# Optimization experiments

Measured on AMD Instinct MI355X. Metric: run time of the kernel, lower is better.

The kernel has to match this reference:

```python
import jax, jax.numpy as jnp
import numpy as np

N = 50000      # nodes
E = 800000     # edges
IN = 256       # in_dim
HID = 64       # num_hidden
H0 = 4         # heads[0]
H1 = 1         # heads[1]
OUT1 = HID * H0  # 256, last GATConv out_feats
C = 64         # num_classes
NEG_SLOPE = 0.2


def setup_inputs() -> dict:
    ks = jax.random.split(jax.random.key(0), 13)
    s = 0.05
    return {
        "x":   jax.random.normal(ks[0], (N, IN), jnp.float32),
        "src": jax.random.randint(ks[1], (E,), 0, N, jnp.int32),
        "dst": jax.random.randint(ks[2], (E,), 0, N, jnp.int32),
        # layer 0: GATConv(IN, HID, H0)
        "W0":  jax.random.normal(ks[3], (IN, H0 * HID), jnp.float32) * s,
        "al0": jax.random.normal(ks[4], (H0, HID), jnp.float32) * s,
        "ar0": jax.random.normal(ks[5], (H0, HID), jnp.float32) * s,
        "b0":  jnp.zeros((H0 * HID,), jnp.float32),
        # layer 1: GATConv(H0*HID, OUT1, H1), residual (identity since in == H1*OUT1)
        "W1":  jax.random.normal(ks[6], (H0 * HID, H1 * OUT1), jnp.float32) * s,
        "al1": jax.random.normal(ks[7], (H1, OUT1), jnp.float32) * s,
        "ar1": jax.random.normal(ks[8], (H1, OUT1), jnp.float32) * s,
        "b1":  jnp.zeros((H1 * OUT1,), jnp.float32),
        # final classifier Linear(OUT1, C)
        "Wl":  jax.random.normal(ks[9], (OUT1, C), jnp.float32) * s,
        "bl":  jnp.zeros((C,), jnp.float32),
    }


def gat_conv(h, src, dst, W, al, ar, b, heads, out, residual, act):
    # ft: projected per-head features [N, H, D]
    ft = (h @ W).reshape(-1, heads, out)
    el = jnp.sum(ft * al, axis=-1)          # [N, H]
    er = jnp.sum(ft * ar, axis=-1)          # [N, H]
    e = jax.nn.leaky_relu(el[src] + er[dst], NEG_SLOPE)  # [E, H]
    # edge softmax grouped by destination node
    emax = jax.ops.segment_max(e, dst, num_segments=N)
    a = jnp.exp(e - emax[dst])
    asum = jax.ops.segment_sum(a, dst, num_segments=N)
    alpha = a / asum[dst]                   # [E, H]
    msg = alpha[:, :, None] * ft[src]       # [E, H, D]
    rst = jax.ops.segment_sum(msg, dst, num_segments=N)  # [N, H, D]
    if residual:  # identity residual (in_feats == heads*out)
        rst = rst + h.reshape(-1, heads, out)
    rst = rst + b.reshape(1, heads, out)
    if act is not None:
        rst = act(rst)
    return rst


def reference(x, src, dst, W0, al0, ar0, b0, W1, al1, ar1, b1, Wl, bl):
    h = gat_conv(x, src, dst, W0, al0, ar0, b0, H0, HID, False, jax.nn.elu)
    h = h.reshape(N, -1)                    # flatten(1) -> [N, H0*HID]
    h = gat_conv(h, src, dst, W1, al1, ar1, b1, H1, OUT1, True, None)
    h = h.mean(axis=1)                      # mean over heads -> [N, OUT1]
    logits = h @ Wl + bl
    return (logits, h)
```

## Files before the change

### kernel.cpp

```cpp
#include <hip/hip_runtime.h>
#include <hip/hip_bf16.h>
#include <stdint.h>

#define NNODES 50000
#define NEDGES 800000
#define CH     256
#define NCLS   64

typedef __attribute__((ext_vector_type(8))) short  short8;
typedef __attribute__((ext_vector_type(4))) float  floatx4;

__device__ __forceinline__ float bf2f(unsigned short u) {
    union { unsigned int i; float f; } v; v.i = ((unsigned int)u) << 16; return v.f;
}
__device__ __forceinline__ unsigned short f2bf(float f) {
    union { float f; unsigned int i; } v; v.f = f;
    unsigned int x = v.i;
    return (unsigned short)((x + 0x7fffu + ((x >> 16) & 1u)) >> 16);
}

__global__ void k_setup(const float* __restrict__ W0, const float* __restrict__ W1,
                        const float* __restrict__ Wl,
                        unsigned short* __restrict__ w0t, unsigned short* __restrict__ w1t,
                        unsigned short* __restrict__ wlt, int* __restrict__ deg) {
    int i = blockIdx.x * 256 + threadIdx.x;
    if (i < 65536) {
        int r = i >> 8, c = i & 255;
        w0t[c * 256 + r] = f2bf(W0[i]);
    } else if (i < 131072) {
        int j = i - 65536;
        int r = j >> 8, c = j & 255;
        w1t[c * 256 + r] = f2bf(W1[j]);
    } else if (i < 147456) {
        int j = i - 131072;
        int r = j >> 6, c = j & 63;
        wlt[c * 256 + r] = f2bf(Wl[j]);
    } else if (i < 147456 + NNODES) {
        deg[i - 147456] = 0;
    }
}

__global__ void k_hist(const int* __restrict__ dst, int* __restrict__ deg) {
    int e = blockIdx.x * 256 + threadIdx.x;
    if (e < NEDGES) {
        int d = dst[e];
        if ((unsigned)d < NNODES) atomicAdd(&deg[d], 1);
    }
}

__global__ void k_scan1(const int* __restrict__ in, int* __restrict__ out,
                        int* __restrict__ part, int n) {
    __shared__ int sm[256];
    int i = blockIdx.x * 256 + threadIdx.x;
    int v = (i < n) ? in[i] : 0;
    sm[threadIdx.x] = v;
    __syncthreads();
    for (int off = 1; off < 256; off <<= 1) {
        int t = (threadIdx.x >= (unsigned)off) ? sm[threadIdx.x - off] : 0;
        __syncthreads();
        sm[threadIdx.x] += t;
        __syncthreads();
    }
    if (i < n) out[i] = sm[threadIdx.x];
    if (threadIdx.x == 255) part[blockIdx.x] = sm[255];
}

__global__ void k_scan3(const int* __restrict__ scn, const int* __restrict__ deg,
                        const int* __restrict__ part, int* __restrict__ offs,
                        int* __restrict__ cursor, int n) {
    int i = blockIdx.x * 256 + threadIdx.x;
    if (i < n) {
        int add = (blockIdx.x > 0) ? part[blockIdx.x - 1] : 0;
        int o = scn[i] - deg[i] + add;
        offs[i] = o; cursor[i] = o;
    }
}

__global__ void k_scatter(const int* __restrict__ dst, const int* __restrict__ src,
                          int* __restrict__ cursor, int* __restrict__ esrc) {
    int e = blockIdx.x * 256 + threadIdx.x;
    if (e < NEDGES) {
        int d = dst[e];
        if ((unsigned)d < NNODES) {
            int p = atomicAdd(&cursor[d], 1);
            if ((unsigned)p < NEDGES) esrc[p] = src[e];
        }
    }
}

template<int BN, bool ABF16, bool OUTF32>
__global__ __launch_bounds__(256) void k_gemm(const void* __restrict__ Av,
                                              const unsigned short* __restrict__ BT,
                                              const float* __restrict__ bias,
                                              float* __restrict__ Cf,
                                              unsigned short* __restrict__ Cb,
                                              int M, int N) {
    constexpr int BK  = 32;
    constexpr int NT  = BN / 16;
    constexpr int LDA = BK + 8;
    __shared__ unsigned short As[128][LDA];
    __shared__ unsigned short Bs[BN][LDA];
    const int t  = threadIdx.x;
    const int w  = t >> 6, l = t & 63;
    const int lm = l & 15, lk = (l >> 4) * 8;
    const int m0 = blockIdx.x * 128;
    const int n0 = blockIdx.y * BN;
    const float* Af = (const float*)Av;
    const unsigned short* Ab = (const unsigned short*)Av;

    floatx4 acc[2][NT];
#pragma unroll
    for (int mt = 0; mt < 2; ++mt)
#pragma unroll
        for (int nt = 0; nt < NT; ++nt) acc[mt][nt] = (floatx4)0.0f;

    for (int k0 = 0; k0 < 256; k0 += BK) {
        if (ABF16) {
#pragma unroll
            for (int p = 0; p < 2; ++p) {
                int chunk = t + p * 256;
                int r = chunk >> 2, cc = (chunk & 3) * 8;
                int row = m0 + r;
                uint4 val = make_uint4(0, 0, 0, 0);
                if (row < M) val = *(const uint4*)(Ab + (size_t)row * 256 + k0 + cc);
                *(uint4*)&As[r][cc] = val;
            }
        } else {
#pragma unroll
            for (int p = 0; p < 4; ++p) {
                int chunk = t + p * 256;
                int r = chunk >> 3, cc = (chunk & 7) * 4;
                int row = m0 + r;
                float4 v = make_float4(0.f, 0.f, 0.f, 0.f);
                if (row < M) v = *(const float4*)(Af + (size_t)row * 256 + k0 + cc);
                ushort4 o; o.x = f2bf(v.x); o.y = f2bf(v.y); o.z = f2bf(v.z); o.w = f2bf(v.w);
                *(ushort4*)&As[r][cc] = o;
            }
        }
#pragma unroll
        for (int p = 0; p < (BN * 4) / 256; ++p) {
            int chunk = t + p * 256;
            int r = chunk >> 2, cc = (chunk & 3) * 8;
            *(uint4*)&Bs[r][cc] = *(const uint4*)(BT + (size_t)(n0 + r) * 256 + k0 + cc);
        }
        __syncthreads();
        short8 af0 = *(const short8*)&As[w * 32 +      lm][lk];
        short8 af1 = *(const short8*)&As[w * 32 + 16 + lm][lk];
#pragma unroll
        for (int nt = 0; nt < NT; ++nt) {
            short8 bf = *(const short8*)&Bs[nt * 16 + lm][lk];
            acc[0][nt] = __builtin_amdgcn_mfma_f32_16x16x32_bf16(af0, bf, acc[0][nt], 0, 0, 0);
            acc[1][nt] = __builtin_amdgcn_mfma_f32_16x16x32_bf16(af1, bf, acc[1][nt], 0, 0, 0);
        }
        __syncthreads();
    }
#pragma unroll
    for (int mt = 0; mt < 2; ++mt)
#pragma unroll
        for (int j = 0; j < 4; ++j) {
            int row = m0 + w * 32 + mt * 16 + (l >> 4) * 4 + j;
            if (row < M) {
#pragma unroll
                for (int nt = 0; nt < NT; ++nt) {
                    int gcol = n0 + nt * 16 + lm;
                    float v = acc[mt][nt][j];
                    if (bias) v += bias[gcol];
                    if (OUTF32) Cf[(size_t)row * N + gcol] = v;
                    else        Cb[(size_t)row * N + gcol] = f2bf(v);
                }
            }
        }
}

template<int H>
__global__ void k_el_er(const unsigned short* __restrict__ ft,
                        const float* __restrict__ al, const float* __restrict__ ar,
                        float* __restrict__ el, float* __restrict__ er) {
    constexpr int D = CH / H;
    constexpr int G = D / 4;
    int n = blockIdx.x * 4 + (threadIdx.x >> 6);
    int l = threadIdx.x & 63;
    int c = 4 * l;
    int h = c / D;
    ushort4 f = *(const ushort4*)(ft + (size_t)n * CH + c);
    float4 a = *(const float4*)(al + c);
    float4 b = *(const float4*)(ar + c);
    float f0 = bf2f(f.x), f1 = bf2f(f.y), f2 = bf2f(f.z), f3 = bf2f(f.w);
    float sl = f0 * a.x + f1 * a.y + f2 * a.z + f3 * a.w;
    float sr = f0 * b.x + f1 * b.y + f2 * b.z + f3 * b.w;
#pragma unroll
    for (int m = 1; m < G; m <<= 1) {
        sl += __shfl_xor(sl, m, 64);
        sr += __shfl_xor(sr, m, 64);
    }
    if ((l & (G - 1)) == 0) {
        el[n * H + h] = sl;
        er[n * H + h] = sr;
    }
}

template<int H, bool ELU, bool RESID>
__global__ __launch_bounds__(256) void k_agg(const unsigned short* __restrict__ ft,
                      const float* __restrict__ el, const float* __restrict__ er,
                      const int* __restrict__ offs, const int* __restrict__ deg,
                      const int* __restrict__ esrc,
                      const unsigned short* __restrict__ resid16,
                      const float* __restrict__ bias,
                      unsigned short* __restrict__ out_bf,
                      float* __restrict__ out_f) {
    constexpr int D = CH / H;
    constexpr int SLOTS = 64 / H;
    __shared__ float swgt[4][64];
    __shared__ int   ssrc[4][64];
    int w = threadIdx.x >> 6;
    int n = blockIdx.x * 4 + w;
    int l = threadIdx.x & 63;
    int c = 4 * l;
    int h = c / D;
    int slot = l / H, head = l & (H - 1);
    float ern1 = er[n * H + head];
    int st = offs[n], dg = deg[n];
    if (st < 0 || dg < 0 || st > NEDGES || dg > NEDGES - st) dg = 0;
    float a0 = 0.f, a1 = 0.f, a2 = 0.f, a3 = 0.f, ssum = 0.f;

    for (int i = 0; i < dg; i += SLOTS) {
        int idx = i + slot;
        int sv = 0; float wv = 0.f;
        if (idx < dg) {
            sv = esrc[st + idx];
            float xv = el[sv * H + head] + ern1;
            xv = (xv > 0.f) ? xv : 0.2f * xv;
            xv = fminf(xv, 60.f);
            wv = __expf(xv);
        }
        swgt[w][slot * H + head] = wv;
        if (head == 0) ssrc[w][slot] = sv;
        int jmax = dg - i; if (jmax > SLOTS) jmax = SLOTS;
        int j = 0;
        for (; j + 4 <= jmax; j += 4) {
            float w0 = swgt[w][(j + 0) * H + h], w1 = swgt[w][(j + 1) * H + h];
            float w2 = swgt[w][(j + 2) * H + h], w3 = swgt[w][(j + 3) * H + h];
            int s0 = ssrc[w][j + 0], s1 = ssrc[w][j + 1];
            int s2 = ssrc[w][j + 2], s3 = ssrc[w][j + 3];
            ushort4 f0 = *(const ushort4*)(ft + (size_t)s0 * CH + c);
            ushort4 f1 = *(const ushort4*)(ft + (size_t)s1 * CH + c);
            ushort4 f2 = *(const ushort4*)(ft + (size_t)s2 * CH + c);
            ushort4 f3 = *(const ushort4*)(ft + (size_t)s3 * CH + c);
            ssum += (w0 + w1) + (w2 + w3);
            a0 += w0 * bf2f(f0.x) + w1 * bf2f(f1.x) + w2 * bf2f(f2.x) + w3 * bf2f(f3.x);
            a1 += w0 * bf2f(f0.y) + w1 * bf2f(f1.y) + w2 * bf2f(f2.y) + w3 * bf2f(f3.y);
            a2 += w0 * bf2f(f0.z) + w1 * bf2f(f1.z) + w2 * bf2f(f2.z) + w3 * bf2f(f3.z);
            a3 += w0 * bf2f(f0.w) + w1 * bf2f(f1.w) + w2 * bf2f(f2.w) + w3 * bf2f(f3.w);
        }
        for (; j < jmax; ++j) {
            float wj = swgt[w][j * H + h];
            int sj = ssrc[w][j];
            ushort4 f = *(const ushort4*)(ft + (size_t)sj * CH + c);
            ssum += wj;
            a0 += wj * bf2f(f.x); a1 += wj * bf2f(f.y);
            a2 += wj * bf2f(f.z); a3 += wj * bf2f(f.w);
        }
    }
    float inv = (ssum > 1e-30f) ? 1.0f / ssum : 0.0f;
    a0 *= inv; a1 *= inv; a2 *= inv; a3 *= inv;
    if (RESID) {
        ushort4 r = *(const ushort4*)(resid16 + (size_t)n * CH + c);
        a0 += bf2f(r.x); a1 += bf2f(r.y); a2 += bf2f(r.z); a3 += bf2f(r.w);
    }
    {
        float4 b = *(const float4*)(bias + c);
        a0 += b.x; a1 += b.y; a2 += b.z; a3 += b.w;
    }
    if (ELU) {
        a0 = (a0 > 0.f) ? a0 : __expf(a0) - 1.f;
        a1 = (a1 > 0.f) ? a1 : __expf(a1) - 1.f;
        a2 = (a2 > 0.f) ? a2 : __expf(a2) - 1.f;
        a3 = (a3 > 0.f) ? a3 : __expf(a3) - 1.f;
    }
    if (out_bf) {
        ushort4 ov; ov.x = f2bf(a0); ov.y = f2bf(a1); ov.z = f2bf(a2); ov.w = f2bf(a3);
        *(ushort4*)(out_bf + (size_t)n * CH + c) = ov;
    }
    if (out_f) {
        *(float4*)(out_f + (size_t)n * CH + c) = make_float4(a0, a1, a2, a3);
    }
}


extern "C" void kernel_launch(void* const* d_in, const int* in_sizes, int n_in,
                              void* d_out, int out_size, void* d_ws, size_t ws_size,
                              hipStream_t stream) {
    const float* x   = (const float*)d_in[0];
    const int*   src = (const int*)d_in[1];
    const int*   dst = (const int*)d_in[2];
    const float* W0  = (const float*)d_in[3];
    const float* al0 = (const float*)d_in[4];
    const float* ar0 = (const float*)d_in[5];
    const float* b0  = (const float*)d_in[6];
    const float* W1  = (const float*)d_in[7];
    const float* al1 = (const float*)d_in[8];
    const float* ar1 = (const float*)d_in[9];
    const float* b1  = (const float*)d_in[10];
    const float* Wl  = (const float*)d_in[11];
    const float* bl  = (const float*)d_in[12];

    float* out_logits = (float*)d_out;
    float* out_h      = out_logits + (size_t)NNODES * NCLS;

    char* ob = (char*)d_out;
    size_t oo = 0;
    auto oalloc = [&](size_t b) { char* p = ob + oo; oo += (b + 255) & ~(size_t)255; return p; };
    int*   esrc = (int*)oalloc((size_t)NEDGES * 4);
    int*   deg  = (int*)oalloc((size_t)NNODES * 4);
    int*   offs = (int*)oalloc((size_t)NNODES * 4);
    int*   curs = (int*)oalloc((size_t)NNODES * 4);
    int*   scn  = (int*)oalloc((size_t)NNODES * 4);
    float* el0  = (float*)oalloc((size_t)NNODES * 4 * 4);
    float* er0  = (float*)oalloc((size_t)NNODES * 4 * 4);
    float* el1  = (float*)oalloc((size_t)NNODES * 4);
    float* er1  = (float*)oalloc((size_t)NNODES * 4);

    char* ws = (char*)d_ws;
    size_t o = 0;
    auto alloc = [&](size_t b) { char* p = ws + o; o += (b + 255) & ~(size_t)255; return p; };
    unsigned short* ft   = (unsigned short*)alloc((size_t)NNODES * CH * 2);
    unsigned short* h0bf = (unsigned short*)alloc((size_t)NNODES * CH * 2);
    unsigned short* w0t  = (unsigned short*)alloc(256 * 256 * 2);
    unsigned short* w1t  = (unsigned short*)alloc(256 * 256 * 2);
    unsigned short* wlt  = (unsigned short*)alloc(64 * 256 * 2);
    int*            part = (int*)alloc(1024);
    int*            dmy  = (int*)alloc(256);
    unsigned short* h1bf = nullptr;
    if (o + (size_t)NNODES * CH * 2 <= ws_size) {
        h1bf = (unsigned short*)alloc((size_t)NNODES * CH * 2);
    }

    k_setup<<<(147456 + NNODES + 255) / 256, 256, 0, stream>>>(W0, W1, Wl, w0t, w1t, wlt, deg);
    k_hist<<<(NEDGES + 255) / 256, 256, 0, stream>>>(dst, deg);
    int nb = (NNODES + 255) / 256;
    k_scan1<<<nb, 256, 0, stream>>>(deg, scn, part, NNODES);
    k_scan1<<<1, 256, 0, stream>>>(part, part, dmy, nb);
    k_scan3<<<nb, 256, 0, stream>>>(scn, deg, part, offs, curs, NNODES);
    k_scatter<<<(NEDGES + 255) / 256, 256, 0, stream>>>(dst, src, curs, esrc);

    int gm = (NNODES + 127) / 128;
    k_gemm<128, false, false><<<dim3(gm, 2), 256, 0, stream>>>(x, w0t, nullptr,
                                                               nullptr, ft, NNODES, CH);
    k_el_er<4><<<NNODES / 4, 256, 0, stream>>>(ft, al0, ar0, el0, er0);
    k_agg<4, true, false><<<NNODES / 4, 256, 0, stream>>>(ft, el0, er0, offs, deg, esrc,
                                                          nullptr, b0, h0bf, nullptr);
    k_gemm<128, true, false><<<dim3(gm, 2), 256, 0, stream>>>(h0bf, w1t, nullptr,
                                                              nullptr, ft, NNODES, CH);
    k_el_er<1><<<NNODES / 4, 256, 0, stream>>>(ft, al1, ar1, el1, er1);
    k_agg<1, false, true><<<NNODES / 4, 256, 0, stream>>>(ft, el1, er1, offs, deg, esrc,
                                                          h0bf, b1, h1bf, out_h);
    if (h1bf) {
        k_gemm<64, true, true><<<dim3(gm, 1), 256, 0, stream>>>(h1bf, wlt, bl,
                                                                out_logits, nullptr, NNODES, NCLS);
    } else {
        k_gemm<64, false, true><<<dim3(gm, 1), 256, 0, stream>>>(out_h, wlt, bl,
                                                                 out_logits, nullptr, NNODES, NCLS);
    }
}
```

Before: 413.0 us.

## Precompute edge attention weights in separate kernel and broadcast via readlane in aggregation

Adds a per-edge kernel that computes exp(leaky_relu(el[src]+er[dst])) into a buffer, with destination indices filled during the el/er pass. The aggregation kernel then loads precomputed weights and broadcasts source indices and weights across the wavefront with readlane/shuffle instead of LDS staging. This aims to shorten the gather loop's dependency chain and remove LDS traffic, at the cost of extra kernel launches and extra global memory writes and reads of edge buffers placed in output scratch space.

```diff
diff --git a/kernel.cpp b/kernel.cpp
--- a/kernel.cpp
+++ b/kernel.cpp
@@ -175,7 +175,9 @@
 template<int H>
 __global__ void k_el_er(const unsigned short* __restrict__ ft,
                         const float* __restrict__ al, const float* __restrict__ ar,
-                        float* __restrict__ el, float* __restrict__ er) {
+                        float* __restrict__ el, float* __restrict__ er,
+                        const int* __restrict__ offs, const int* __restrict__ deg,
+                        int* __restrict__ edst) {
     constexpr int D = CH / H;
     constexpr int G = D / 4;
     int n = blockIdx.x * 4 + (threadIdx.x >> 6);
@@ -197,71 +199,132 @@
         el[n * H + h] = sl;
         er[n * H + h] = sr;
     }
+    if (edst) {
+        int st = offs[n], dg = deg[n];
+        if (st >= 0 && dg >= 0 && st <= NEDGES && dg <= NEDGES - st) {
+            for (int i = l; i < dg; i += 64) edst[st + i] = n;
+        }
+    }
+}
+
+template<int H>
+__global__ void k_wedge(const int* __restrict__ esrc, const int* __restrict__ edst,
+                        const float* __restrict__ el, const float* __restrict__ er,
+                        float* __restrict__ wout) {
+    int t = blockIdx.x * 256 + threadIdx.x;
+    if (t < NEDGES * H) {
+        int e = (H == 1) ? t : (t >> 2);
+        int h = (H == 1) ? 0 : (t & 3);
+        int s = esrc[e], d = edst[e];
+        float x = el[s * H + h] + er[d * H + h];
+        x = (x > 0.f) ? x : 0.2f * x;
+        x = fminf(x, 60.f);
+        wout[t] = __expf(x);
+    }
 }
 
 template<int H, bool ELU, bool RESID>
-__global__ __launch_bounds__(256) void k_agg(const unsigned short* __restrict__ ft,
-                      const float* __restrict__ el, const float* __restrict__ er,
-                      const int* __restrict__ offs, const int* __restrict__ deg,
-                      const int* __restrict__ esrc,
-                      const unsigned short* __restrict__ resid16,
-                      const float* __restrict__ bias,
-                      unsigned short* __restrict__ out_bf,
-                      float* __restrict__ out_f) {
-    constexpr int D = CH / H;
-    constexpr int SLOTS = 64 / H;
-    __shared__ float swgt[4][64];
-    __shared__ int   ssrc[4][64];
+__global__ __launch_bounds__(256) void k_agg2(
+        const unsigned short* __restrict__ ft,
+        const float* __restrict__ wedge,
+        const int* __restrict__ offs, const int* __restrict__ deg,
+        const int* __restrict__ esrc,
+        const unsigned short* __restrict__ resid16,
+        const float* __restrict__ bias,
+        unsigned short* __restrict__ out_bf,
+        float* __restrict__ out_f) {
     int w = threadIdx.x >> 6;
     int n = blockIdx.x * 4 + w;
     int l = threadIdx.x & 63;
     int c = 4 * l;
-    int h = c / D;
-    int slot = l / H, head = l & (H - 1);
-    float ern1 = er[n * H + head];
-    int st = offs[n], dg = deg[n];
+    int st = __builtin_amdgcn_readfirstlane(offs[n]);
+    int dg = __builtin_amdgcn_readfirstlane(deg[n]);
     if (st < 0 || dg < 0 || st > NEDGES || dg > NEDGES - st) dg = 0;
-    float a0 = 0.f, a1 = 0.f, a2 = 0.f, a3 = 0.f, ssum = 0.f;
-
-    for (int i = 0; i < dg; i += SLOTS) {
-        int idx = i + slot;
-        int sv = 0; float wv = 0.f;
-        if (idx < dg) {
-            sv = esrc[st + idx];
-            float xv = el[sv * H + head] + ern1;
-            xv = (xv > 0.f) ? xv : 0.2f * xv;
-            xv = fminf(xv, 60.f);
-            wv = __expf(xv);
-        }
-        swgt[w][slot * H + head] = wv;
-        if (head == 0) ssrc[w][slot] = sv;
-        int jmax = dg - i; if (jmax > SLOTS) jmax = SLOTS;
-        int j = 0;
-        for (; j + 4 <= jmax; j += 4) {
-            float w0 = swgt[w][(j + 0) * H + h], w1 = swgt[w][(j + 1) * H + h];
-            float w2 = swgt[w][(j + 2) * H + h], w3 = swgt[w][(j + 3) * H + h];
-            int s0 = ssrc[w][j + 0], s1 = ssrc[w][j + 1];
-            int s2 = ssrc[w][j + 2], s3 = ssrc[w][j + 3];
-            ushort4 f0 = *(const ushort4*)(ft + (size_t)s0 * CH + c);
-            ushort4 f1 = *(const ushort4*)(ft + (size_t)s1 * CH + c);
-            ushort4 f2 = *(const ushort4*)(ft + (size_t)s2 * CH + c);
-            ushort4 f3 = *(const ushort4*)(ft + (size_t)s3 * CH + c);
-            ssum += (w0 + w1) + (w2 + w3);
-            a0 += w0 * bf2f(f0.x) + w1 * bf2f(f1.x) + w2 * bf2f(f2.x) + w3 * bf2f(f3.x);
-            a1 += w0 * bf2f(f0.y) + w1 * bf2f(f1.y) + w2 * bf2f(f2.y) + w3 * bf2f(f3.y);
-            a2 += w0 * bf2f(f0.z) + w1 * bf2f(f1.z) + w2 * bf2f(f2.z) + w3 * bf2f(f3.z);
-            a3 += w0 * bf2f(f0.w) + w1 * bf2f(f1.w) + w2 * bf2f(f2.w) + w3 * bf2f(f3.w);
-        }
-        for (; j < jmax; ++j) {
-            float wj = swgt[w][j * H + h];
-            int sj = ssrc[w][j];
-            ushort4 f = *(const ushort4*)(ft + (size_t)sj * CH + c);
-            ssum += wj;
-            a0 += wj * bf2f(f.x); a1 += wj * bf2f(f.y);
-            a2 += wj * bf2f(f.z); a3 += wj * bf2f(f.w);
-        }
-    }
-    float inv = (ssum > 1e-30f) ? 1.0f / ssum : 0.0f;
+    float a0 = 0.f, a1 = 0.f, a2 = 0.f, a3 = 0.f, wsum = 0.f;
+    const unsigned short* ftc = ft + c;
+
+    if (H == 1) {
+        for (int i = 0; i < dg; i += 64) {
+            int idx = i + l;
+            int sv = 0; float wv = 0.f;
+            if (idx < dg) {
+                sv = esrc[st + idx];
+                wv = wedge[st + idx];
+            }
+            wsum += wv;
+            int jmax = dg - i; if (jmax > 64) jmax = 64;
+            int j = 0;
+            for (; j + 4 <= jmax; j += 4) {
+                int s0 = __builtin_amdgcn_readlane(sv, j + 0);
+                int s1 = __builtin_amdgcn_readlane(sv, j + 1);
+                int s2 = __builtin_amdgcn_readlane(sv, j + 2);
+                int s3 = __builtin_amdgcn_readlane(sv, j + 3);
+                float w0 = __int_as_float(__builtin_amdgcn_readlane(__float_as_int(wv), j + 0));
+                float w1 = __int_as_float(__builtin_amdgcn_readlane(__float_as_int(wv), j + 1));
+                float w2 = __int_as_float(__builtin_amdgcn_readlane(__float_as_int(wv), j + 2));
+                float w3 = __int_as_float(__builtin_amdgcn_readlane(__float_as_int(wv), j + 3));
+                ushort4 f0 = *(const ushort4*)(ftc + (size_t)s0 * CH);
+                ushort4 f1 = *(const ushort4*)(ftc + (size_t)s1 * CH);
+                ushort4 f2 = *(const ushort4*)(ftc + (size_t)s2 * CH);
+                ushort4 f3 = *(const ushort4*)(ftc + (size_t)s3 * CH);
+                a0 += w0 * bf2f(f0.x) + w1 * bf2f(f1.x) + w2 * bf2f(f2.x) + w3 * bf2f(f3.x);
+                a1 += w0 * bf2f(f0.y) + w1 * bf2f(f1.y) + w2 * bf2f(f2.y) + w3 * bf2f(f3.y);
+                a2 += w0 * bf2f(f0.z) + w1 * bf2f(f1.z) + w2 * bf2f(f2.z) + w3 * bf2f(f3.z);
+                a3 += w0 * bf2f(f0.w) + w1 * bf2f(f1.w) + w2 * bf2f(f2.w) + w3 * bf2f(f3.w);
+            }
+            for (; j < jmax; ++j) {
+                int s0 = __builtin_amdgcn_readlane(sv, j);
+                float w0 = __int_as_float(__builtin_amdgcn_readlane(__float_as_int(wv), j));
+                ushort4 f0 = *(const ushort4*)(ftc + (size_t)s0 * CH);
+                a0 += w0 * bf2f(f0.x); a1 += w0 * bf2f(f0.y);
+                a2 += w0 * bf2f(f0.z); a3 += w0 * bf2f(f0.w);
+            }
+        }
+#pragma unroll
+        for (int m = 1; m < 64; m <<= 1) wsum += __shfl_xor(wsum, m, 64);
+    } else {
+        int h = l >> 4;
+        for (int i = 0; i < dg; i += 16) {
+            int slot = i + (l >> 2);
+            int sv = 0; float wv = 0.f;
+            if (slot < dg) {
+                sv = esrc[st + slot];
+                wv = wedge[(size_t)(st + i) * 4 + l];
+            }
+            wsum += wv;
+            int jmax = dg - i; if (jmax > 16) jmax = 16;
+            int j = 0;
+            for (; j + 4 <= jmax; j += 4) {
+                int s0 = __builtin_amdgcn_readlane(sv, 4 * (j + 0));
+                int s1 = __builtin_amdgcn_readlane(sv, 4 * (j + 1));
+                int s2 = __builtin_amdgcn_readlane(sv, 4 * (j + 2));
+                int s3 = __builtin_amdgcn_readlane(sv, 4 * (j + 3));
+                float w0 = __shfl(wv, 4 * (j + 0) + h, 64);
+                float w1 = __shfl(wv, 4 * (j + 1) + h, 64);
+                float w2 = __shfl(wv, 4 * (j + 2) + h, 64);
+                float w3 = __shfl(wv, 4 * (j + 3) + h, 64);
+                ushort4 f0 = *(const ushort4*)(ftc + (size_t)s0 * CH);
+                ushort4 f1 = *(const ushort4*)(ftc + (size_t)s1 * CH);
+                ushort4 f2 = *(const ushort4*)(ftc + (size_t)s2 * CH);
+                ushort4 f3 = *(const ushort4*)(ftc + (size_t)s3 * CH);
+                a0 += w0 * bf2f(f0.x) + w1 * bf2f(f1.x) + w2 * bf2f(f2.x) + w3 * bf2f(f3.x);
+                a1 += w0 * bf2f(f0.y) + w1 * bf2f(f1.y) + w2 * bf2f(f2.y) + w3 * bf2f(f3.y);
+                a2 += w0 * bf2f(f0.z) + w1 * bf2f(f1.z) + w2 * bf2f(f2.z) + w3 * bf2f(f3.z);
+                a3 += w0 * bf2f(f0.w) + w1 * bf2f(f1.w) + w2 * bf2f(f2.w) + w3 * bf2f(f3.w);
+            }
+            for (; j < jmax; ++j) {
+                int s0 = __builtin_amdgcn_readlane(sv, 4 * j);
+                float w0 = __shfl(wv, 4 * j + h, 64);
+                ushort4 f0 = *(const ushort4*)(ftc + (size_t)s0 * CH);
+                a0 += w0 * bf2f(f0.x); a1 += w0 * bf2f(f0.y);
+                a2 += w0 * bf2f(f0.z); a3 += w0 * bf2f(f0.w);
+            }
+        }
+#pragma unroll
+        for (int m = 4; m < 64; m <<= 1) wsum += __shfl_xor(wsum, m, 64);
+        wsum = __shfl(wsum, h, 64);
+    }
+    float inv = (wsum > 1e-30f) ? 1.0f / wsum : 0.0f;
     a0 *= inv; a1 *= inv; a2 *= inv; a3 *= inv;
     if (RESID) {
         ushort4 r = *(const ushort4*)(resid16 + (size_t)n * CH + c);
@@ -319,6 +382,13 @@
     float* er0  = (float*)oalloc((size_t)NNODES * 4 * 4);
     float* el1  = (float*)oalloc((size_t)NNODES * 4);
     float* er1  = (float*)oalloc((size_t)NNODES * 4);
+    float* wedge1 = (float*)oalloc((size_t)NEDGES * 4);
+
+    char* hb = (char*)out_h;
+    size_t ho = 0;
+    auto halloc = [&](size_t b) { char* p = hb + ho; ho += (b + 255) & ~(size_t)255; return p; };
+    int*   edst   = (int*)halloc((size_t)NEDGES * 4);
+    float* wedge4 = (float*)halloc((size_t)NEDGES * 4 * 4);
 
     char* ws = (char*)d_ws;
     size_t o = 0;
@@ -346,14 +416,16 @@
     int gm = (NNODES + 127) / 128;
     k_gemm<128, false, false><<<dim3(gm, 2), 256, 0, stream>>>(x, w0t, nullptr,
                                                                nullptr, ft, NNODES, CH);
-    k_el_er<4><<<NNODES / 4, 256, 0, stream>>>(ft, al0, ar0, el0, er0);
-    k_agg<4, true, false><<<NNODES / 4, 256, 0, stream>>>(ft, el0, er0, offs, deg, esrc,
-                                                          nullptr, b0, h0bf, nullptr);
+    k_el_er<4><<<NNODES / 4, 256, 0, stream>>>(ft, al0, ar0, el0, er0, offs, deg, edst);
+    k_wedge<4><<<(NEDGES * 4 + 255) / 256, 256, 0, stream>>>(esrc, edst, el0, er0, wedge4);
+    k_agg2<4, true, false><<<NNODES / 4, 256, 0, stream>>>(ft, wedge4, offs, deg, esrc,
+                                                           nullptr, b0, h0bf, nullptr);
     k_gemm<128, true, false><<<dim3(gm, 2), 256, 0, stream>>>(h0bf, w1t, nullptr,
                                                               nullptr, ft, NNODES, CH);
-    k_el_er<1><<<NNODES / 4, 256, 0, stream>>>(ft, al1, ar1, el1, er1);
-    k_agg<1, false, true><<<NNODES / 4, 256, 0, stream>>>(ft, el1, er1, offs, deg, esrc,
-                                                          h0bf, b1, h1bf, out_h);
+    k_el_er<1><<<NNODES / 4, 256, 0, stream>>>(ft, al1, ar1, el1, er1, nullptr, nullptr, nullptr);
+    k_wedge<1><<<(NEDGES + 255) / 256, 256, 0, stream>>>(esrc, edst, el1, er1, wedge1);
+    k_agg2<1, false, true><<<NNODES / 4, 256, 0, stream>>>(ft, wedge1, offs, deg, esrc,
+                                                           h0bf, b1, h1bf, out_h);
     if (h1bf) {
         k_gemm<64, true, true><<<dim3(gm, 1), 256, 0, stream>>>(h1bf, wlt, bl,
                                                                 out_logits, nullptr, NNODES, NCLS);
```

New measurement: 427.8 us. 3.6% more time.
